# Kernel optimization log

Hardware: AMD Instinct MI355X
Metric: run time of the kernel (lower is better)

## Reference

```python
import jax, jax.numpy as jnp
import numpy as np

N, E, Z, H = 16384, 131072, 128, 8
ZH = Z // H
CUTOFF = 5.0


def _dense(key, din, dout, bias=True):
    kw, kb = jax.random.split(key)
    W = (jax.random.normal(kw, (din, dout), jnp.float32) / np.sqrt(din)).astype(jnp.float32)
    if bias:
        return W, jnp.zeros((dout,), jnp.float32)
    return W


def setup_inputs() -> dict:
    key = jax.random.key(0)
    ks = jax.random.split(key, 24)
    edge_index = jax.random.randint(ks[0], (2, E), 0, N)
    h_N_1_Z = jax.random.normal(ks[1], (N, 1, Z), jnp.float32)
    mu_N_L2_Z = jax.random.normal(ks[2], (N, 3, Z), jnp.float32) * 0.1
    ev = jax.random.normal(ks[3], (E, 3), jnp.float32)
    edge_vec_E_3 = ev / jnp.linalg.norm(ev, axis=-1, keepdims=True)
    edge_emb_E_Z = jax.random.normal(ks[4], (E, Z), jnp.float32)
    edge_weight_E = jax.random.uniform(ks[5], (E,), jnp.float32, 0.5, CUTOFF)
    deg = jax.ops.segment_sum(jnp.ones((E,), jnp.float32), edge_index[1], num_segments=N)
    num_edges_expanded_E = deg[edge_index[1]]
    inp = dict(edge_index=edge_index, h_N_1_Z=h_N_1_Z, mu_N_L2_Z=mu_N_L2_Z,
               edge_vec_E_3=edge_vec_E_3, edge_emb_E_Z=edge_emb_E_Z,
               edge_weight_E=edge_weight_E, num_edges_expanded_E=num_edges_expanded_E)
    inp['W_q'], inp['b_q'] = _dense(ks[6], Z, Z)
    inp['W_k'], inp['b_k'] = _dense(ks[7], Z, Z)
    inp['W_gs1'], inp['b_gs1'] = _dense(ks[8], Z, Z)
    inp['W_gs2'], inp['b_gs2'] = _dense(ks[9], Z, 3 * Z)
    inp['W_gv1'], inp['b_gv1'] = _dense(ks[10], Z, Z)
    inp['W_gv2'], inp['b_gv2'] = _dense(ks[11], Z, 3 * Z)
    inp['W_phik'], inp['b_phik'] = _dense(ks[12], Z, Z)
    inp['W_re'], inp['b_re'] = _dense(ks[13], Z, 3 * Z)
    inp['W_vq'] = _dense(ks[14], Z, Z, bias=False)   # vecq_w, no bias
    inp['W_vk0'] = _dense(ks[15], Z, Z, bias=False)  # veck_w[0] (lmax=1), no bias
    inp['W_lin'], inp['b_lin'] = _dense(ks[16], Z, Z)  # lin_w_linear
    inp['W_eu1'], inp['b_eu1'] = _dense(ks[17], Z, Z)  # edge_attr_up MLP [Z,Z,Z]
    inp['W_eu2'], inp['b_eu2'] = _dense(ks[18], Z, Z)
    return inp


def reference(edge_index, h_N_1_Z, mu_N_L2_Z, edge_vec_E_3, edge_emb_E_Z,
              edge_weight_E, num_edges_expanded_E,
              W_q, b_q, W_k, b_k, W_gs1, b_gs1, W_gs2, b_gs2,
              W_gv1, b_gv1, W_gv2, b_gv2, W_phik, b_phik, W_re, b_re,
              W_vq, W_vk0, W_lin, b_lin, W_eu1, b_eu1, W_eu2, b_eu2):
    silu = jax.nn.silu
    src, dst = edge_index[0], edge_index[1]  # messages j->i aggregated at dst=i
    hs = h_N_1_Z[:, 0]                        # (N, Z); layernorm='' -> identity
    q = (hs @ W_q + b_q).reshape(N, H, ZH)
    k = (hs @ W_k + b_k).reshape(N, H, ZH)
    x3 = silu(hs @ W_gs1 + b_gs1) @ W_gs2 + b_gs2    # gamma_s: (N, 3Z)
    val3 = silu(hs @ W_gv1 + b_gv1) @ W_gv2 + b_gv2  # gamma_v: (N, 3Z)
    r_attn = silu(edge_emb_E_Z @ W_phik + b_phik).reshape(E, H, ZH)
    r_ij = edge_emb_E_Z @ W_re + b_re                # (E, 3Z)

    # per-edge multi-head attention with segment softmax over target node
    logits = jnp.sum(q[dst] * k[src] * r_attn, axis=-1)        # (E, H)
    m = jax.ops.segment_max(logits, dst, num_segments=N)
    ex = jnp.exp(logits - m[dst])
    den = jax.ops.segment_sum(ex, dst, num_segments=N)
    attn = ex / den[dst]
    attn = attn * (jnp.sqrt(num_edges_expanded_E)[:, None] / np.float32(np.sqrt(Z)))

    sea = (attn[..., None] * val3[src].reshape(E, H, 3 * ZH)).reshape(E, 3 * Z)
    cut = 0.5 * (jnp.cos(jnp.pi * edge_weight_E / CUTOFF) + 1.0) * (edge_weight_E < CUTOFF)
    x_ij = cut[:, None] * sea * (x3[src] * r_ij)               # (E, 3Z)
    o_s, o_d, o_t = x_ij[:, :Z], x_ij[:, Z:2 * Z], x_ij[:, 2 * Z:]
    dmu_ij = o_d[:, None, :] * edge_vec_E_3[..., None] + o_t[:, None, :] * mu_N_L2_Z[src]  # (E,3,Z)

    h_out = h_N_1_Z + jax.ops.segment_sum(o_s, dst, num_segments=N)[:, None, :]
    mu_out = mu_N_L2_Z + jax.ops.segment_sum(dmu_ij, dst, num_segments=N)

    # edge update (sep_vecj, lmax=1 -> single degree block)
    w1 = jnp.einsum('nlz,ze->nle', mu_out, W_vq)
    w2 = jnp.einsum('nlz,ze->nle', mu_out, W_vk0)
    w1_d = jnp.sum(w1[dst] * edge_vec_E_3[..., None], axis=1)  # (E, evec)
    w2_d = jnp.sum(w2[src] * edge_vec_E_3[..., None], axis=1)
    w_dot = jnp.tanh((w1_d * w2_d) @ W_lin + b_lin)            # gated='gatedt'
    f_up = silu(edge_emb_E_Z @ W_eu1 + b_eu1) @ W_eu2 + b_eu2  # edge_attr_up MLP
    df_ij = edge_emb_E_Z + f_up * w_dot
    return h_out, mu_out, df_ij
```

## Files before the change

kernel.cpp:

```cpp
#include <hip/hip_runtime.h>
#include <math.h>

#define NN 16384
#define EE 131072
#define ZZ 128
#define HH 8

typedef short bf16x8 __attribute__((ext_vector_type(8)));
typedef float f32x4 __attribute__((ext_vector_type(4)));
typedef unsigned short ushort4v __attribute__((ext_vector_type(4)));
typedef unsigned short ushort8v __attribute__((ext_vector_type(8)));

__device__ __forceinline__ float silu_f(float x) { return x / (1.0f + __expf(-x)); }

__device__ __forceinline__ unsigned short f2bf(float x) {
    unsigned u = __float_as_uint(x);
    unsigned r = (u >> 16) & 1u;
    u += 0x7fffu + r;
    return (unsigned short)(u >> 16);
}
__device__ __forceinline__ float bf2f(unsigned short x) {
    return __uint_as_float(((unsigned)x) << 16);
}

__device__ __forceinline__ f32x4 mfma16(bf16x8 a, bf16x8 b, f32x4 c) {
    return __builtin_amdgcn_mfma_f32_16x16x32_bf16(a, b, c, 0, 0, 0);
}

__device__ __forceinline__ void stageB(const unsigned short* Wt, char* lB, int t) {
    const uint4* Wg = (const uint4*)Wt;
#pragma unroll
    for (int i = 0; i < 8; ++i) {
        const int cid = t + i * 256;
        const int n = cid >> 4, c16 = cid & 15;
        *(uint4*)(lB + ((n * 256 + c16 * 16) ^ ((n & 7) << 4))) = Wg[cid];
    }
}

struct WPrep {
    const float* w[13];
    int P[13];
    int tile0[14];
};

__global__ __launch_bounds__(128) void prep_weights(WPrep wp, unsigned short* wt) {
    int b = blockIdx.x, wi = 0;
    while (b >= wp.tile0[wi + 1]) ++wi;
    const int cg = (b - wp.tile0[wi]) * 128;
    const float* w = wp.w[wi];
    unsigned short* o = wt + (size_t)wp.tile0[wi] * 16384;
    const int P = wp.P[wi];
    const int t = threadIdx.x;
    for (int k0 = 0; k0 < 128; k0 += 8) {
        ushort8v v;
#pragma unroll
        for (int j = 0; j < 8; ++j) v[j] = f2bf(w[(size_t)(k0 + j) * P + cg + t]);
        *(ushort8v*)(o + (size_t)(cg + t) * 128 + k0) = v;
    }
}

struct BPrep {
    const float* b[13];
    int off[14];
};

__global__ __launch_bounds__(256) void prep_bias(BPrep bp, float* bcat) {
    const int idx = blockIdx.x * 256 + threadIdx.x;
    if (idx >= 2432) return;
    int wi = 0;
    while (idx >= bp.off[wi + 1]) ++wi;
    bcat[idx] = bp.b[wi] ? bp.b[wi][idx - bp.off[wi]] : 0.f;
}

template <int ACT, int INBF, int DUMP>
__global__ __launch_bounds__(256, 2) void mm_bf16(
    const void* __restrict__ Av, const unsigned short* __restrict__ Wt,
    const float* __restrict__ bias, unsigned short* __restrict__ C,
    const unsigned short* __restrict__ aux, unsigned short* __restrict__ dumpA,
    int P, int As)
{
    __shared__ uint4 lA4[2048];
    __shared__ uint4 lB4[2048];
    char* lA = (char*)lA4;
    char* lB = (char*)lB4;
    const int t = threadIdx.x;
    const size_t row0 = (size_t)blockIdx.x * 128;
    const int cg = blockIdx.y * 128;
    if (INBF) {
        const uint4* Ag = (const uint4*)((const unsigned short*)Av + row0 * As);
        const int rs = As >> 3;
#pragma unroll
        for (int i = 0; i < 8; ++i) {
            const int chunk = t + i * 256;
            const int r = chunk >> 4, c16 = chunk & 15;
            *(uint4*)(lA + ((r * 256 + c16 * 16) ^ ((r & 7) << 4))) = Ag[r * rs + c16];
        }
    } else {
        const float4* Ag = (const float4*)((const float*)Av + row0 * As);
        const int rs = As >> 2;
#pragma unroll
        for (int i = 0; i < 16; ++i) {
            const int f4 = t + i * 256;
            const int r = f4 >> 5, c4 = f4 & 31;
            const float4 v = Ag[r * rs + c4];
            ushort4v bb;
            bb.x = f2bf(v.x); bb.y = f2bf(v.y); bb.z = f2bf(v.z); bb.w = f2bf(v.w);
            *(ushort4v*)(lA + ((r * 256 + c4 * 8) ^ ((r & 7) << 4))) = bb;
        }
    }
    stageB(Wt + (size_t)cg * 128, lB, t);
    __syncthreads();
    if (DUMP) {
#pragma unroll
        for (int i = 0; i < 8; ++i) {
            const int ch = t + i * 256;
            const int row = ch >> 4, cpos = ch & 15;
            const uint4 v = *(const uint4*)(lA + ((row * 256 + cpos * 16) ^ ((row & 7) << 4)));
            *(uint4*)(dumpA + (row0 + row) * 128 + cpos * 8) = v;
        }
    }
    const int lane = t & 63, wid = t >> 6;
    const int rbase = (wid >> 1) * 64, cbase = (wid & 1) * 64;
    const int lr = lane & 15, lgp = lane >> 4;
    f32x4 acc[4][4];
#pragma unroll
    for (int i = 0; i < 4; ++i)
#pragma unroll
        for (int j = 0; j < 4; ++j) acc[i][j] = (f32x4){0.f, 0.f, 0.f, 0.f};
#pragma unroll
    for (int ks = 0; ks < 4; ++ks) {
        bf16x8 av[4], bv[4];
#pragma unroll
        for (int mt = 0; mt < 4; ++mt) {
            const int r = rbase + mt * 16 + lr;
            av[mt] = *(const bf16x8*)(lA + ((r * 256 + ks * 64 + lgp * 16) ^ ((r & 7) << 4)));
        }
#pragma unroll
        for (int nt = 0; nt < 4; ++nt) {
            const int c = cbase + nt * 16 + lr;
            bv[nt] = *(const bf16x8*)(lB + ((c * 256 + ks * 64 + lgp * 16) ^ ((c & 7) << 4)));
        }
#pragma unroll
        for (int mt = 0; mt < 4; ++mt)
#pragma unroll
            for (int nt = 0; nt < 4; ++nt)
                acc[mt][nt] = mfma16(av[mt], bv[nt], acc[mt][nt]);
    }
    __syncthreads();
#pragma unroll
    for (int nt = 0; nt < 4; ++nt) {
        const int col = cbase + nt * 16 + lr;
        const int gcol = cg + col;
        const float b = bias[gcol];
#pragma unroll
        for (int mt = 0; mt < 4; ++mt) {
#pragma unroll
            for (int j = 0; j < 4; ++j) {
                const int row = rbase + mt * 16 + lgp * 4 + j;
                float v = acc[mt][nt][j] + b;
                if (ACT == 1) v = silu_f(v);
                if (ACT == 2) v = v * bf2f(aux[(row0 + row) * (size_t)P + gcol]);
                *(unsigned short*)(lB + ((row * 256 + col * 2) ^ ((row & 7) << 4))) = f2bf(v);
            }
        }
    }
    __syncthreads();
#pragma unroll
    for (int i = 0; i < 8; ++i) {
        const int ch = t + i * 256;
        const int row = ch >> 4, cpos = ch & 15;
        const uint4 v = *(const uint4*)(lB + ((row * 256 + cpos * 16) ^ ((row & 7) << 4)));
        *(uint4*)(C + (row0 + row) * (size_t)P + cg + cpos * 8) = v;
    }
}

__global__ __launch_bounds__(256) void attn_kernel(
    const int* __restrict__ row_start, const int* __restrict__ perm,
    const int* __restrict__ src, const unsigned short* __restrict__ qkb,
    const unsigned short* __restrict__ rab, const float* __restrict__ ewt,
    float* __restrict__ attnw)
{
    const int t = threadIdx.x;
    const int n = blockIdx.x * 4 + (t >> 6);
    const int lane = t & 63;
    const int el = lane >> 3, h = lane & 7;
    const int beg = row_start[n], end = row_start[n + 1];
    if (beg == end) return;
    const ushort8v q0 = *(const ushort8v*)(qkb + (size_t)n * 256 + h * 16);
    const ushort8v q1 = *(const ushort8v*)(qkb + (size_t)n * 256 + h * 16 + 8);
    float m = -1e30f, den = 0.f;
    for (int i0 = beg; i0 < end; i0 += 8) {
        const int i = i0 + el;
        const bool valid = i < end;
        const int e = perm[valid ? i : beg];
        const int s = src[e];
        const ushort8v k0 = *(const ushort8v*)(qkb + (size_t)s * 256 + 128 + h * 16);
        const ushort8v k1 = *(const ushort8v*)(qkb + (size_t)s * 256 + 128 + h * 16 + 8);
        const ushort8v r0 = *(const ushort8v*)(rab + (size_t)e * 128 + h * 16);
        const ushort8v r1 = *(const ushort8v*)(rab + (size_t)e * 128 + h * 16 + 8);
        float lgv = 0.f;
#pragma unroll
        for (int j = 0; j < 8; ++j) lgv += bf2f(q0[j]) * bf2f(k0[j]) * bf2f(r0[j]);
#pragma unroll
        for (int j = 0; j < 8; ++j) lgv += bf2f(q1[j]) * bf2f(k1[j]) * bf2f(r1[j]);
        if (!valid) lgv = -1e30f;
        else attnw[(size_t)e * 8 + h] = lgv;
        float cm = lgv;
        cm = fmaxf(cm, __shfl_xor(cm, 8));
        cm = fmaxf(cm, __shfl_xor(cm, 16));
        cm = fmaxf(cm, __shfl_xor(cm, 32));
        const float nm = fmaxf(m, cm);
        float ex = valid ? __expf(lgv - nm) : 0.f;
        float cd = ex;
        cd += __shfl_xor(cd, 8);
        cd += __shfl_xor(cd, 16);
        cd += __shfl_xor(cd, 32);
        den = den * __expf(m - nm) + cd;
        m = nm;
    }
    const float sc = sqrtf((float)(end - beg)) * 0.08838834764831845f / den;
    for (int i0 = beg; i0 < end; i0 += 8) {
        const int i = i0 + el;
        if (i >= end) continue;
        const int e = perm[i];
        const float w = ewt[e];
        const float cut = (w < 5.0f) ? 0.5f * (cosf(w * 0.62831853071795864f) + 1.0f) : 0.0f;
        const float lgv = attnw[(size_t)e * 8 + h];
        attnw[(size_t)e * 8 + h] = __expf(lgv - m) * sc * cut;
    }
}

__global__ __launch_bounds__(256, 4) void combine_mfma(
    const unsigned short* __restrict__ embb, const unsigned short* __restrict__ Wt_re,
    const float* __restrict__ bre, const float* __restrict__ attnw,
    unsigned short* __restrict__ osb, unsigned short* __restrict__ odb,
    unsigned short* __restrict__ otb)
{
    __shared__ uint4 lA4[2048];
    __shared__ float attnS[128 * 8];
    char* lA = (char*)lA4;
    const int t = threadIdx.x;
    const size_t e0 = (size_t)blockIdx.x * 128;
    {
        const uint4* Ag = (const uint4*)(embb + e0 * 128);
#pragma unroll
        for (int i = 0; i < 8; ++i) {
            const int chunk = t + i * 256;
            const int r = chunk >> 4, c16 = chunk & 15;
            *(uint4*)(lA + ((r * 256 + c16 * 16) ^ ((r & 7) << 4))) = Ag[chunk];
        }
    }
    ((float4*)attnS)[t] = ((const float4*)(attnw + e0 * 8))[t];
    __syncthreads();
    const int lane = t & 63, wid = t >> 6;
    const int rbase = (wid >> 1) * 64, cbase = (wid & 1) * 64;
    const int lr = lane & 15, lgp = lane >> 4;
    unsigned short* bufs[3] = {osb, odb, otb};
    for (int cg3 = 0; cg3 < 3; ++cg3) {
        const unsigned short* Wp = Wt_re + (size_t)cg3 * 16384;
        f32x4 acc[4][4];
#pragma unroll
        for (int i = 0; i < 4; ++i)
#pragma unroll
            for (int j = 0; j < 4; ++j) acc[i][j] = (f32x4){0.f, 0.f, 0.f, 0.f};
#pragma unroll
        for (int ks = 0; ks < 4; ++ks) {
            bf16x8 av[4], bv[4];
#pragma unroll
            for (int mt = 0; mt < 4; ++mt) {
                const int r = rbase + mt * 16 + lr;
                av[mt] = *(const bf16x8*)(lA + ((r * 256 + ks * 64 + lgp * 16) ^ ((r & 7) << 4)));
            }
#pragma unroll
            for (int nt = 0; nt < 4; ++nt)
                bv[nt] = *(const bf16x8*)(Wp + (size_t)(cbase + nt * 16 + lr) * 128 + ks * 32 + lgp * 8);
#pragma unroll
            for (int mt = 0; mt < 4; ++mt)
#pragma unroll
                for (int nt = 0; nt < 4; ++nt)
                    acc[mt][nt] = mfma16(bv[nt], av[mt], acc[mt][nt]);
        }
        unsigned short* buf = bufs[cg3];
        const int cgo = cg3 * 128;
#pragma unroll
        for (int mt = 0; mt < 4; ++mt) {
            const int row = rbase + mt * 16 + lr;
            const float* aS = attnS + row * 8;
#pragma unroll
            for (int nt = 0; nt < 4; ++nt) {
                const int col0 = cbase + nt * 16 + lgp * 4;
                const int gcol = cgo + col0;
                const float coef = aS[gcol / 48];
                const float4 b4 = *(const float4*)(bre + gcol);
                ushort4v st;
                st.x = f2bf((acc[mt][nt][0] + b4.x) * coef);
                st.y = f2bf((acc[mt][nt][1] + b4.y) * coef);
                st.z = f2bf((acc[mt][nt][2] + b4.z) * coef);
                st.w = f2bf((acc[mt][nt][3] + b4.w) * coef);
                *(ushort4v*)(buf + (e0 + row) * 128 + col0) = st;
            }
        }
    }
}

__global__ __launch_bounds__(256, 3) void wdot_fused(
    const unsigned short* __restrict__ w12, const float* __restrict__ ev,
    const int* __restrict__ src, const int* __restrict__ dst,
    const unsigned short* __restrict__ Wt_lin, const float* __restrict__ bl,
    const unsigned short* __restrict__ embb, const unsigned short* __restrict__ fup,
    float* __restrict__ df)
{
    __shared__ uint4 lA4[2048];
    char* lA = (char*)lA4;
    const int t = threadIdx.x;
    const size_t e0 = (size_t)blockIdx.x * 128;
#pragma unroll
    for (int i = 0; i < 8; ++i) {
        const int chunk = t + i * 256;
        const int r = chunk >> 4, c8 = chunk & 15;
        const size_t e = e0 + r;
        const int s = src[e], d = dst[e];
        const float e0v = ev[e * 3 + 0], e1v = ev[e * 3 + 1], e2v = ev[e * 3 + 2];
        const ushort8v a0 = *(const ushort8v*)(w12 + ((size_t)d * 3 + 0) * 256 + c8 * 8);
        const ushort8v a1 = *(const ushort8v*)(w12 + ((size_t)d * 3 + 1) * 256 + c8 * 8);
        const ushort8v a2 = *(const ushort8v*)(w12 + ((size_t)d * 3 + 2) * 256 + c8 * 8);
        const ushort8v c0 = *(const ushort8v*)(w12 + ((size_t)s * 3 + 0) * 256 + 128 + c8 * 8);
        const ushort8v c1 = *(const ushort8v*)(w12 + ((size_t)s * 3 + 1) * 256 + 128 + c8 * 8);
        const ushort8v c2 = *(const ushort8v*)(w12 + ((size_t)s * 3 + 2) * 256 + 128 + c8 * 8);
        ushort8v o;
#pragma unroll
        for (int j = 0; j < 8; ++j) {
            const float av = e0v * bf2f(a0[j]) + e1v * bf2f(a1[j]) + e2v * bf2f(a2[j]);
            const float bv = e0v * bf2f(c0[j]) + e1v * bf2f(c1[j]) + e2v * bf2f(c2[j]);
            o[j] = f2bf(av * bv);
        }
        *(ushort8v*)(lA + ((r * 256 + c8 * 16) ^ ((r & 7) << 4))) = o;
    }
    __syncthreads();
    const int lane = t & 63, wid = t >> 6;
    const int rbase = (wid >> 1) * 64, cbase = (wid & 1) * 64;
    const int lr = lane & 15, lgp = lane >> 4;
    f32x4 acc[4][4];
#pragma unroll
    for (int i = 0; i < 4; ++i)
#pragma unroll
        for (int j = 0; j < 4; ++j) acc[i][j] = (f32x4){0.f, 0.f, 0.f, 0.f};
#pragma unroll
    for (int ks = 0; ks < 4; ++ks) {
        bf16x8 av[4], bv[4];
#pragma unroll
        for (int mt = 0; mt < 4; ++mt) {
            const int r = rbase + mt * 16 + lr;
            av[mt] = *(const bf16x8*)(lA + ((r * 256 + ks * 64 + lgp * 16) ^ ((r & 7) << 4)));
        }
#pragma unroll
        for (int nt = 0; nt < 4; ++nt)
            bv[nt] = *(const bf16x8*)(Wt_lin + (size_t)(cbase + nt * 16 + lr) * 128 + ks * 32 + lgp * 8);
#pragma unroll
        for (int mt = 0; mt < 4; ++mt)
#pragma unroll
            for (int nt = 0; nt < 4; ++nt)
                acc[mt][nt] = mfma16(bv[nt], av[mt], acc[mt][nt]);
    }
#pragma unroll
    for (int mt = 0; mt < 4; ++mt) {
        const int row = rbase + mt * 16 + lr;
#pragma unroll
        for (int nt = 0; nt < 4; ++nt) {
            const int col0 = cbase + nt * 16 + lgp * 4;
            const float4 b4 = *(const float4*)(bl + col0);
            const size_t base = (e0 + row) * 128 + col0;
            const ushort4v em = *(const ushort4v*)(embb + base);
            const ushort4v fu = *(const ushort4v*)(fup + base);
            float4 o;
            o.x = bf2f(em.x) + bf2f(fu.x) * tanhf(acc[mt][nt][0] + b4.x);
            o.y = bf2f(em.y) + bf2f(fu.y) * tanhf(acc[mt][nt][1] + b4.y);
            o.z = bf2f(em.z) + bf2f(fu.z) * tanhf(acc[mt][nt][2] + b4.z);
            o.w = bf2f(em.w) + bf2f(fu.w) * tanhf(acc[mt][nt][3] + b4.w);
            *(float4*)(df + base) = o;
        }
    }
}

__global__ __launch_bounds__(256) void hist_kernel(const int* __restrict__ dst, int* __restrict__ counts) {
    const int e = blockIdx.x * 256 + threadIdx.x;
    atomicAdd(&counts[dst[e]], 1);
}

__global__ __launch_bounds__(256) void scan_kernel(const int* __restrict__ counts,
                                                   int* __restrict__ row_start,
                                                   int* __restrict__ cursor) {
    __shared__ int part[256];
    const int t = threadIdx.x;
    const int base = t * 64;
    int local[64];
    int s = 0;
#pragma unroll
    for (int i = 0; i < 64; ++i) { local[i] = s; s += counts[base + i]; }
    part[t] = s;
    __syncthreads();
    for (int off = 1; off < 256; off <<= 1) {
        int v = (t >= off) ? part[t - off] : 0;
        __syncthreads();
        part[t] += v;
        __syncthreads();
    }
    const int prev = (t == 0) ? 0 : part[t - 1];
#pragma unroll
    for (int i = 0; i < 64; ++i) {
        const int v = prev + local[i];
        row_start[base + i] = v;
        cursor[base + i] = v;
    }
    if (t == 255) row_start[NN] = prev + s;
}

__global__ __launch_bounds__(256) void fill_kernel(const int* __restrict__ dst,
                                                   int* __restrict__ cursor,
                                                   int* __restrict__ perm) {
    const int e = blockIdx.x * 256 + threadIdx.x;
    const int p = atomicAdd(&cursor[dst[e]], 1);
    perm[p] = e;
}

__global__ __launch_bounds__(256) void gather_kernel(
    const int* __restrict__ row_start, const int* __restrict__ perm,
    const int* __restrict__ src, const unsigned short* __restrict__ osb,
    const unsigned short* __restrict__ odb, const unsigned short* __restrict__ otb,
    const unsigned short* __restrict__ xv, const float* __restrict__ ev,
    const float* __restrict__ h_in, const float* __restrict__ mu_in,
    float* __restrict__ h_out, float* __restrict__ mu_out)
{
    const int n = blockIdx.x * 2 + (threadIdx.x >> 7);
    const int t = threadIdx.x & 127;
    const int beg = row_start[n], end = row_start[n + 1];
    float hacc = h_in[(size_t)n * 128 + t];
    float m0 = mu_in[(size_t)n * 384 + t];
    float m1 = mu_in[(size_t)n * 384 + 128 + t];
    float m2 = mu_in[(size_t)n * 384 + 256 + t];
    for (int i = beg; i < end; ++i) {
        const int e = perm[i];
        const int s = src[e];
        const float e0 = ev[e * 3 + 0], e1 = ev[e * 3 + 1], e2 = ev[e * 3 + 2];
        const unsigned short* xp = xv + (size_t)s * 384 + t;
        const float osv = bf2f(osb[(size_t)e * 128 + t]) * bf2f(xp[0]);
        const float odv = bf2f(odb[(size_t)e * 128 + t]) * bf2f(xp[128]);
        const float otv = bf2f(otb[(size_t)e * 128 + t]) * bf2f(xp[256]);
        const float* msp = mu_in + (size_t)s * 384 + t;
        hacc += osv;
        m0 += odv * e0 + otv * msp[0];
        m1 += odv * e1 + otv * msp[128];
        m2 += odv * e2 + otv * msp[256];
    }
    h_out[(size_t)n * 128 + t] = hacc;
    mu_out[(size_t)n * 384 + t] = m0;
    mu_out[(size_t)n * 384 + 128 + t] = m1;
    mu_out[(size_t)n * 384 + 256 + t] = m2;
}

extern "C" void kernel_launch(void* const* d_in, const int* in_sizes, int n_in,
                              void* d_out, int out_size, void* d_ws, size_t ws_size,
                              hipStream_t stream) {
    const int* eidx = (const int*)d_in[0];
    const int* src = eidx;
    const int* dst = eidx + EE;
    const float* h_in  = (const float*)d_in[1];
    const float* mu_in = (const float*)d_in[2];
    const float* ev    = (const float*)d_in[3];
    const float* emb   = (const float*)d_in[4];
    const float* ewt   = (const float*)d_in[5];
    const float* W_q   = (const float*)d_in[7];  const float* b_q   = (const float*)d_in[8];
    const float* W_k   = (const float*)d_in[9];  const float* b_k   = (const float*)d_in[10];
    const float* W_gs1 = (const float*)d_in[11]; const float* b_gs1 = (const float*)d_in[12];
    const float* W_gs2 = (const float*)d_in[13]; const float* b_gs2 = (const float*)d_in[14];
    const float* W_gv1 = (const float*)d_in[15]; const float* b_gv1 = (const float*)d_in[16];
    const float* W_gv2 = (const float*)d_in[17]; const float* b_gv2 = (const float*)d_in[18];
    const float* W_phik= (const float*)d_in[19]; const float* b_phik= (const float*)d_in[20];
    const float* W_re  = (const float*)d_in[21]; const float* b_re  = (const float*)d_in[22];
    const float* W_vq  = (const float*)d_in[23];
    const float* W_vk0 = (const float*)d_in[24];
    const float* W_lin = (const float*)d_in[25]; const float* b_lin = (const float*)d_in[26];
    const float* W_eu1 = (const float*)d_in[27]; const float* b_eu1 = (const float*)d_in[28];
    const float* W_eu2 = (const float*)d_in[29]; const float* b_eu2 = (const float*)d_in[30];

    float* out    = (float*)d_out;
    float* h_out  = out;
    float* mu_out = out + (size_t)NN * ZZ;
    float* df     = out + (size_t)NN * ZZ * 4;

    const size_t NZ = (size_t)NN * ZZ, N3Z = (size_t)NN * 3 * ZZ, EZ = (size_t)EE * ZZ;
    const size_t EH = (size_t)EE * HH;
    char* p = (char*)d_ws;
    unsigned short* qkb   = (unsigned short*)p; p += NZ * 2 * 2;
    unsigned short* tmpn2 = (unsigned short*)p; p += NZ * 2 * 2;
    unsigned short* x3b   = (unsigned short*)p; p += N3Z * 2;
    unsigned short* xv    = (unsigned short*)p; p += N3Z * 2;
    unsigned short* w12   = (unsigned short*)p; p += N3Z * 2 * 2;
    unsigned short* embb  = (unsigned short*)p; p += EZ * 2;
    unsigned short* rab   = (unsigned short*)p; p += EZ * 2;
    unsigned short* tmpe  = (unsigned short*)p; p += EZ * 2;
    unsigned short* fup   = (unsigned short*)p; p += EZ * 2;
    unsigned short* osb   = (unsigned short*)p; p += EZ * 2;
    unsigned short* odb   = (unsigned short*)p; p += EZ * 2;
    unsigned short* otb   = (unsigned short*)p; p += EZ * 2;
    float* attnw          = (float*)p;          p += EH * 4;
    unsigned short* wt    = (unsigned short*)p; p += 2432 * 128 * 2;
    float* bcat           = (float*)p;          p += 2432 * 4;
    int* counts           = (int*)p;            p += NN * 4;
    int* cursor           = (int*)p;            p += NN * 4;
    int* row_start        = (int*)p;            p += (NN + 1) * 4;
    int* perm             = (int*)p;            p += EE * 4;

    const float* wsrc[13] = {W_q, W_k, W_gs1, W_gv1, W_gs2, W_gv2, W_phik,
                             W_re, W_vq, W_vk0, W_lin, W_eu1, W_eu2};
    const float* bsrc[13] = {b_q, b_k, b_gs1, b_gv1, b_gs2, b_gv2, b_phik,
                             b_re, nullptr, nullptr, b_lin, b_eu1, b_eu2};
    const int Ps[13] = {128, 128, 128, 128, 384, 384, 128, 384, 128, 128, 128, 128, 128};
    WPrep wp; BPrep bp;
    int tiles = 0;
    for (int i = 0; i < 13; ++i) {
        wp.w[i] = wsrc[i]; wp.P[i] = Ps[i]; wp.tile0[i] = tiles;
        bp.b[i] = bsrc[i]; bp.off[i] = tiles * 128;
        tiles += Ps[i] / 128;
    }
    wp.tile0[13] = tiles; bp.off[13] = tiles * 128;
    unsigned short* wT[13]; const float* bC[13];
    for (int i = 0; i < 13; ++i) { wT[i] = wt + (size_t)wp.tile0[i] * 16384; bC[i] = bcat + bp.off[i]; }

    dim3 blk(256);
    prep_weights<<<dim3(tiles), dim3(128), 0, stream>>>(wp, wt);
    prep_bias<<<dim3(10), blk, 0, stream>>>(bp, bcat);
    mm_bf16<0,0,0><<<dim3(NN/128, 2), blk, 0, stream>>>(h_in, wT[0], bC[0], qkb, nullptr, nullptr, 256, 128);
    mm_bf16<1,0,0><<<dim3(NN/128, 2), blk, 0, stream>>>(h_in, wT[2], bC[2], tmpn2, nullptr, nullptr, 256, 128);
    mm_bf16<0,1,0><<<dim3(NN/128, 3), blk, 0, stream>>>(tmpn2, wT[4], bC[4], x3b, nullptr, nullptr, 384, 256);
    mm_bf16<2,1,0><<<dim3(NN/128, 3), blk, 0, stream>>>(tmpn2 + 128, wT[5], bC[5], xv, x3b, nullptr, 384, 256);
    mm_bf16<1,0,1><<<dim3(EE/128, 1), blk, 0, stream>>>(emb, wT[11], bC[11], tmpe, nullptr, embb, 128, 128);
    mm_bf16<0,1,0><<<dim3(EE/128, 1), blk, 0, stream>>>(tmpe, wT[12], bC[12], fup, nullptr, nullptr, 128, 128);
    mm_bf16<1,1,0><<<dim3(EE/128, 1), blk, 0, stream>>>(embb, wT[6], bC[6], rab, nullptr, nullptr, 128, 128);
    hipMemsetAsync(counts, 0, NN * 4, stream);
    hist_kernel<<<dim3(EE/256), blk, 0, stream>>>(dst, counts);
    scan_kernel<<<dim3(1), blk, 0, stream>>>(counts, row_start, cursor);
    fill_kernel<<<dim3(EE/256), blk, 0, stream>>>(dst, cursor, perm);
    attn_kernel<<<dim3(NN/4), blk, 0, stream>>>(row_start, perm, src, qkb, rab, ewt, attnw);
    combine_mfma<<<dim3(EE/128), blk, 0, stream>>>(
        embb, wT[7], bC[7], attnw, osb, odb, otb);
    gather_kernel<<<dim3(NN/2), blk, 0, stream>>>(
        row_start, perm, src, osb, odb, otb, xv, ev, h_in, mu_in, h_out, mu_out);
    mm_bf16<0,0,0><<<dim3(3*NN/128, 2), blk, 0, stream>>>(mu_out, wT[8], bC[8], w12, nullptr, nullptr, 256, 128);
    wdot_fused<<<dim3(EE/128), blk, 0, stream>>>(
        w12, ev, src, dst, wT[10], bC[10], embb, fup, df);
}
```

Baseline: 416.4 us.

## Store per-edge data in dst-sorted order and cast mu to bf16 for gather

The fill kernel now scatters src, edge weight and edge vector into dst-sorted arrays. The attention weights and combine outputs are indexed by sorted position, with combine gathering embedding rows through perm. The gather kernel then streams its per-edge data contiguously and reads a bf16 copy of mu instead of the fp32 one. This trades random per-edge indirection in attention and gather for one indirect row load in combine and a few extra scatter writes. It also drops mu precision to bf16 in the aggregation.

```diff
diff --git a/kernel.cpp b/kernel.cpp
--- a/kernel.cpp
+++ b/kernel.cpp
@@ -70,6 +70,17 @@
     int wi = 0;
     while (idx >= bp.off[wi + 1]) ++wi;
     bcat[idx] = bp.b[wi] ? bp.b[wi][idx - bp.off[wi]] : 0.f;
+}
+
+__global__ __launch_bounds__(256) void prep_mub(const float* __restrict__ mu,
+                                                unsigned short* __restrict__ mub) {
+    const size_t idx = (size_t)blockIdx.x * 256 + threadIdx.x;
+    const float4 a = ((const float4*)mu)[idx * 2];
+    const float4 b = ((const float4*)mu)[idx * 2 + 1];
+    ushort8v v;
+    v[0] = f2bf(a.x); v[1] = f2bf(a.y); v[2] = f2bf(a.z); v[3] = f2bf(a.w);
+    v[4] = f2bf(b.x); v[5] = f2bf(b.y); v[6] = f2bf(b.z); v[7] = f2bf(b.w);
+    *(ushort8v*)(mub + idx * 8) = v;
 }
 
 template <int ACT, int INBF, int DUMP>
@@ -176,8 +187,8 @@
 
 __global__ __launch_bounds__(256) void attn_kernel(
     const int* __restrict__ row_start, const int* __restrict__ perm,
-    const int* __restrict__ src, const unsigned short* __restrict__ qkb,
-    const unsigned short* __restrict__ rab, const float* __restrict__ ewt,
+    const int* __restrict__ srcp, const unsigned short* __restrict__ qkb,
+    const unsigned short* __restrict__ rab, const float* __restrict__ ewp,
     float* __restrict__ attnw)
 {
     const int t = threadIdx.x;
@@ -192,8 +203,9 @@
     for (int i0 = beg; i0 < end; i0 += 8) {
         const int i = i0 + el;
         const bool valid = i < end;
-        const int e = perm[valid ? i : beg];
-        const int s = src[e];
+        const int ii = valid ? i : beg;
+        const int e = perm[ii];
+        const int s = srcp[ii];
         const ushort8v k0 = *(const ushort8v*)(qkb + (size_t)s * 256 + 128 + h * 16);
         const ushort8v k1 = *(const ushort8v*)(qkb + (size_t)s * 256 + 128 + h * 16 + 8);
         const ushort8v r0 = *(const ushort8v*)(rab + (size_t)e * 128 + h * 16);
@@ -204,7 +216,7 @@
 #pragma unroll
         for (int j = 0; j < 8; ++j) lgv += bf2f(q1[j]) * bf2f(k1[j]) * bf2f(r1[j]);
         if (!valid) lgv = -1e30f;
-        else attnw[(size_t)e * 8 + h] = lgv;
+        else attnw[(size_t)i * 8 + h] = lgv;
         float cm = lgv;
         cm = fmaxf(cm, __shfl_xor(cm, 8));
         cm = fmaxf(cm, __shfl_xor(cm, 16));
@@ -222,40 +234,38 @@
     for (int i0 = beg; i0 < end; i0 += 8) {
         const int i = i0 + el;
         if (i >= end) continue;
-        const int e = perm[i];
-        const float w = ewt[e];
+        const float w = ewp[i];
         const float cut = (w < 5.0f) ? 0.5f * (cosf(w * 0.62831853071795864f) + 1.0f) : 0.0f;
-        const float lgv = attnw[(size_t)e * 8 + h];
-        attnw[(size_t)e * 8 + h] = __expf(lgv - m) * sc * cut;
+        const float lgv = attnw[(size_t)i * 8 + h];
+        attnw[(size_t)i * 8 + h] = __expf(lgv - m) * sc * cut;
     }
 }
 
 __global__ __launch_bounds__(256, 4) void combine_mfma(
-    const unsigned short* __restrict__ embb, const unsigned short* __restrict__ Wt_re,
-    const float* __restrict__ bre, const float* __restrict__ attnw,
-    unsigned short* __restrict__ osb, unsigned short* __restrict__ odb,
-    unsigned short* __restrict__ otb)
+    const unsigned short* __restrict__ embb, const int* __restrict__ perm,
+    const unsigned short* __restrict__ Wt_re, const float* __restrict__ bre,
+    const float* __restrict__ attnw, unsigned short* __restrict__ ob)
 {
     __shared__ uint4 lA4[2048];
     __shared__ float attnS[128 * 8];
+    __shared__ int permS[128];
     char* lA = (char*)lA4;
     const int t = threadIdx.x;
     const size_t e0 = (size_t)blockIdx.x * 128;
-    {
-        const uint4* Ag = (const uint4*)(embb + e0 * 128);
-#pragma unroll
-        for (int i = 0; i < 8; ++i) {
-            const int chunk = t + i * 256;
-            const int r = chunk >> 4, c16 = chunk & 15;
-            *(uint4*)(lA + ((r * 256 + c16 * 16) ^ ((r & 7) << 4))) = Ag[chunk];
-        }
-    }
+    if (t < 128) permS[t] = perm[e0 + t];
     ((float4*)attnS)[t] = ((const float4*)(attnw + e0 * 8))[t];
+    __syncthreads();
+#pragma unroll
+    for (int i = 0; i < 8; ++i) {
+        const int chunk = t + i * 256;
+        const int r = chunk >> 4, c16 = chunk & 15;
+        const uint4 v = *(const uint4*)(embb + (size_t)permS[r] * 128 + c16 * 8);
+        *(uint4*)(lA + ((r * 256 + c16 * 16) ^ ((r & 7) << 4))) = v;
+    }
     __syncthreads();
     const int lane = t & 63, wid = t >> 6;
     const int rbase = (wid >> 1) * 64, cbase = (wid & 1) * 64;
     const int lr = lane & 15, lgp = lane >> 4;
-    unsigned short* bufs[3] = {osb, odb, otb};
     for (int cg3 = 0; cg3 < 3; ++cg3) {
         const unsigned short* Wp = Wt_re + (size_t)cg3 * 16384;
         f32x4 acc[4][4];
@@ -280,7 +290,6 @@
                 for (int nt = 0; nt < 4; ++nt)
                     acc[mt][nt] = mfma16(bv[nt], av[mt], acc[mt][nt]);
         }
-        unsigned short* buf = bufs[cg3];
         const int cgo = cg3 * 128;
 #pragma unroll
         for (int mt = 0; mt < 4; ++mt) {
@@ -297,7 +306,7 @@
                 st.y = f2bf((acc[mt][nt][1] + b4.y) * coef);
                 st.z = f2bf((acc[mt][nt][2] + b4.z) * coef);
                 st.w = f2bf((acc[mt][nt][3] + b4.w) * coef);
-                *(ushort4v*)(buf + (e0 + row) * 128 + col0) = st;
+                *(ushort4v*)(ob + (e0 + row) * 384 + gcol) = st;
             }
         }
     }
@@ -415,19 +424,26 @@
     if (t == 255) row_start[NN] = prev + s;
 }
 
-__global__ __launch_bounds__(256) void fill_kernel(const int* __restrict__ dst,
-                                                   int* __restrict__ cursor,
-                                                   int* __restrict__ perm) {
+__global__ __launch_bounds__(256) void fill_kernel(
+    const int* __restrict__ src, const int* __restrict__ dst,
+    const float* __restrict__ ewt, const float* __restrict__ ev,
+    int* __restrict__ cursor, int* __restrict__ perm,
+    int* __restrict__ srcp, float* __restrict__ ewp, float* __restrict__ evp)
+{
     const int e = blockIdx.x * 256 + threadIdx.x;
     const int p = atomicAdd(&cursor[dst[e]], 1);
     perm[p] = e;
+    srcp[p] = src[e];
+    ewp[p] = ewt[e];
+    evp[p * 3 + 0] = ev[e * 3 + 0];
+    evp[p * 3 + 1] = ev[e * 3 + 1];
+    evp[p * 3 + 2] = ev[e * 3 + 2];
 }
 
 __global__ __launch_bounds__(256) void gather_kernel(
-    const int* __restrict__ row_start, const int* __restrict__ perm,
-    const int* __restrict__ src, const unsigned short* __restrict__ osb,
-    const unsigned short* __restrict__ odb, const unsigned short* __restrict__ otb,
-    const unsigned short* __restrict__ xv, const float* __restrict__ ev,
+    const int* __restrict__ row_start, const int* __restrict__ srcp,
+    const unsigned short* __restrict__ ob, const unsigned short* __restrict__ xv,
+    const unsigned short* __restrict__ mub, const float* __restrict__ evp,
     const float* __restrict__ h_in, const float* __restrict__ mu_in,
     float* __restrict__ h_out, float* __restrict__ mu_out)
 {
@@ -439,18 +455,18 @@
     float m1 = mu_in[(size_t)n * 384 + 128 + t];
     float m2 = mu_in[(size_t)n * 384 + 256 + t];
     for (int i = beg; i < end; ++i) {
-        const int e = perm[i];
-        const int s = src[e];
-        const float e0 = ev[e * 3 + 0], e1 = ev[e * 3 + 1], e2 = ev[e * 3 + 2];
+        const int s = srcp[i];
+        const float e0 = evp[i * 3 + 0], e1 = evp[i * 3 + 1], e2 = evp[i * 3 + 2];
+        const unsigned short* op = ob + (size_t)i * 384 + t;
         const unsigned short* xp = xv + (size_t)s * 384 + t;
-        const float osv = bf2f(osb[(size_t)e * 128 + t]) * bf2f(xp[0]);
-        const float odv = bf2f(odb[(size_t)e * 128 + t]) * bf2f(xp[128]);
-        const float otv = bf2f(otb[(size_t)e * 128 + t]) * bf2f(xp[256]);
-        const float* msp = mu_in + (size_t)s * 384 + t;
+        const unsigned short* mp = mub + (size_t)s * 384 + t;
+        const float osv = bf2f(op[0]) * bf2f(xp[0]);
+        const float odv = bf2f(op[128]) * bf2f(xp[128]);
+        const float otv = bf2f(op[256]) * bf2f(xp[256]);
         hacc += osv;
-        m0 += odv * e0 + otv * msp[0];
-        m1 += odv * e1 + otv * msp[128];
-        m2 += odv * e2 + otv * msp[256];
+        m0 += odv * e0 + otv * bf2f(mp[0]);
+        m1 += odv * e1 + otv * bf2f(mp[128]);
+        m2 += odv * e2 + otv * bf2f(mp[256]);
     }
     h_out[(size_t)n * 128 + t] = hacc;
     mu_out[(size_t)n * 384 + t] = m0;
@@ -495,14 +511,13 @@
     unsigned short* tmpn2 = (unsigned short*)p; p += NZ * 2 * 2;
     unsigned short* x3b   = (unsigned short*)p; p += N3Z * 2;
     unsigned short* xv    = (unsigned short*)p; p += N3Z * 2;
+    unsigned short* mub   = (unsigned short*)p; p += N3Z * 2;
     unsigned short* w12   = (unsigned short*)p; p += N3Z * 2 * 2;
     unsigned short* embb  = (unsigned short*)p; p += EZ * 2;
     unsigned short* rab   = (unsigned short*)p; p += EZ * 2;
     unsigned short* tmpe  = (unsigned short*)p; p += EZ * 2;
     unsigned short* fup   = (unsigned short*)p; p += EZ * 2;
-    unsigned short* osb   = (unsigned short*)p; p += EZ * 2;
-    unsigned short* odb   = (unsigned short*)p; p += EZ * 2;
-    unsigned short* otb   = (unsigned short*)p; p += EZ * 2;
+    unsigned short* ob    = (unsigned short*)p; p += EZ * 3 * 2;
     float* attnw          = (float*)p;          p += EH * 4;
     unsigned short* wt    = (unsigned short*)p; p += 2432 * 128 * 2;
     float* bcat           = (float*)p;          p += 2432 * 4;
@@ -510,6 +525,9 @@
     int* cursor           = (int*)p;            p += NN * 4;
     int* row_start        = (int*)p;            p += (NN + 1) * 4;
     int* perm             = (int*)p;            p += EE * 4;
+    int* srcp             = (int*)p;            p += EE * 4;
+    float* ewp            = (float*)p;          p += EE * 4;
+    float* evp            = (float*)p;          p += EE * 12;
 
     const float* wsrc[13] = {W_q, W_k, W_gs1, W_gv1, W_gs2, W_gv2, W_phik,
                              W_re, W_vq, W_vk0, W_lin, W_eu1, W_eu2};
@@ -530,6 +548,7 @@
     dim3 blk(256);
     prep_weights<<<dim3(tiles), dim3(128), 0, stream>>>(wp, wt);
     prep_bias<<<dim3(10), blk, 0, stream>>>(bp, bcat);
+    prep_mub<<<dim3(N3Z / 8 / 256), blk, 0, stream>>>(mu_in, mub);
     mm_bf16<0,0,0><<<dim3(NN/128, 2), blk, 0, stream>>>(h_in, wT[0], bC[0], qkb, nullptr, nullptr, 256, 128);
     mm_bf16<1,0,0><<<dim3(NN/128, 2), blk, 0, stream>>>(h_in, wT[2], bC[2], tmpn2, nullptr, nullptr, 256, 128);
     mm_bf16<0,1,0><<<dim3(NN/128, 3), blk, 0, stream>>>(tmpn2, wT[4], bC[4], x3b, nullptr, nullptr, 384, 256);
@@ -540,12 +559,11 @@
     hipMemsetAsync(counts, 0, NN * 4, stream);
     hist_kernel<<<dim3(EE/256), blk, 0, stream>>>(dst, counts);
     scan_kernel<<<dim3(1), blk, 0, stream>>>(counts, row_start, cursor);
-    fill_kernel<<<dim3(EE/256), blk, 0, stream>>>(dst, cursor, perm);
-    attn_kernel<<<dim3(NN/4), blk, 0, stream>>>(row_start, perm, src, qkb, rab, ewt, attnw);
-    combine_mfma<<<dim3(EE/128), blk, 0, stream>>>(
-        embb, wT[7], bC[7], attnw, osb, odb, otb);
+    fill_kernel<<<dim3(EE/256), blk, 0, stream>>>(src, dst, ewt, ev, cursor, perm, srcp, ewp, evp);
+    attn_kernel<<<dim3(NN/4), blk, 0, stream>>>(row_start, perm, srcp, qkb, rab, ewp, attnw);
+    combine_mfma<<<dim3(EE/128), blk, 0, stream>>>(embb, perm, wT[7], bC[7], attnw, ob);
     gather_kernel<<<dim3(NN/2), blk, 0, stream>>>(
-        row_start, perm, src, osb, odb, otb, xv, ev, h_in, mu_in, h_out, mu_out);
+        row_start, srcp, ob, xv, mub, evp, h_in, mu_in, h_out, mu_out);
     mm_bf16<0,0,0><<<dim3(3*NN/128, 2), blk, 0, stream>>>(mu_out, wT[8], bC[8], w12, nullptr, nullptr, 256, 128);
     wdot_fused<<<dim3(EE/128), blk, 0, stream>>>(
         w12, ev, src, dst, wT[10], bC[10], embb, fup, df);
```

Result: slower. 438.1 us (+5.2%).
